# Performance work log

Measured on AMD Instinct MI355X. Metric: run time of the kernel, lower is better.

## Reference

```python
import jax, jax.numpy as jnp
import numpy as np

N = 524288
L = 16          # num_levels
F = 2           # per_level_dim
T = 1 << 19     # hashmap size per level
BASE, MAXR = 32, 2048
SCALE = np.exp(np.log(MAXR / BASE) / (L - 1))
RES = [int(np.floor(BASE * SCALE ** lv)) + 1 for lv in range(L)]
ACTIVE = 4 * F  # init_active_level * per_level_dim (progressive mask)
D_HID = 64
N_FREQS = 6

_P1 = jnp.uint32(2654435761)
_P2 = jnp.uint32(805459861)
_OFF = jnp.array([[(c >> d) & 1 for d in range(3)] for c in range(8)], dtype=jnp.uint32)  # [8,3]


def setup_inputs() -> dict:
    key = jax.random.key(0)
    ks = jax.random.split(key, 8)
    x = (jax.random.uniform(ks[0], (N, 3)) * 2.0 - 1.0) * 0.999  # inside [-bound, bound]
    v = jax.random.normal(ks[1], (N, 3))
    v = v / jnp.linalg.norm(v, axis=-1, keepdims=True)
    o = jax.random.normal(ks[2], (N, 3))  # unused by forward (kept for signature fidelity)
    table = jax.random.uniform(ks[3], (L, T, F), minval=-1e-4, maxval=1e-4)
    d_in = 3 + 3 * 2 * N_FREQS + L * F  # xyz + fourier + hashgrid = 71
    def lin(k, fi, fo):
        return jax.random.normal(k, (fi, fo)) * np.sqrt(2.0 / fi).astype(np.float32)
    dw1 = lin(ks[4], d_in, D_HID); db1 = jnp.zeros((D_HID,), jnp.float32)
    dw2 = lin(ks[5], D_HID, 1 + D_HID); db2 = jnp.zeros((1 + D_HID,), jnp.float32)
    rw1 = lin(ks[6], D_HID + 9, D_HID); rb1 = jnp.zeros((D_HID,), jnp.float32)
    rw2 = lin(ks[7], D_HID, 3); rb2 = jnp.zeros((3,), jnp.float32)
    return dict(x=x, v=v, o=o, table=table, dw1=dw1, db1=db1, dw2=dw2, db2=db2,
                rw1=rw1, rb1=rb1, rw2=rw2, rb2=rb2)


def hashgrid(x01, table):
    """Multi-res hash encoding with Smoothstep interpolation. x01 in [0,1]^3."""
    feats = []
    for lv in range(L):
        pos = x01 * RES[lv]
        p0 = jnp.floor(pos)
        t = pos - p0
        w = t * t * (3.0 - 2.0 * t)                       # smoothstep weights [N,3]
        corner = p0.astype(jnp.uint32)[:, None, :] + _OFF[None]  # [N,8,3]
        h = (corner[..., 0] ^ (corner[..., 1] * _P1) ^ (corner[..., 2] * _P2)) & jnp.uint32(T - 1)
        cw = jnp.prod(jnp.where(_OFF[None] == 1, w[:, None, :], 1.0 - w[:, None, :]), axis=-1)  # [N,8]
        feats.append(jnp.sum(table[lv][h.astype(jnp.int32)] * cw[..., None], axis=1))  # [N,F]
    return jnp.concatenate(feats, axis=-1)  # [N, L*F]


def fourier(x):
    freqs = 2.0 ** jnp.arange(N_FREQS, dtype=x.dtype)  # log-sampled 2^0..2^5
    ang = x[..., None] * freqs                         # [N,3,6]
    return jnp.concatenate([jnp.sin(ang), jnp.cos(ang)], axis=-1).reshape(x.shape[0], -1)


def sh3(d):
    """Spherical harmonics, degree 3 (levels=3) -> 9 features."""
    xx, yy, zz = d[..., 0], d[..., 1], d[..., 2]
    return jnp.stack([
        0.28209479177387814 * jnp.ones_like(xx),
        -0.4886025119029199 * yy, 0.4886025119029199 * zz, -0.4886025119029199 * xx,
        1.0925484305920792 * xx * yy, -1.0925484305920792 * yy * zz,
        0.9461746957575601 * zz * zz - 0.31539156525252005,
        -1.0925484305920792 * xx * zz,
        0.5462742152960396 * (xx * xx - yy * yy)], axis=-1)


def reference(x, v, o, table, dw1, db1, dw2, db2, rw1, rb1, rw2, rb2):
    x01 = (x + 1.0) * 0.5  # bound = 1.0
    grid = hashgrid(x01, table)
    mask = (jnp.arange(L * F) < ACTIVE).astype(grid.dtype)  # progressive level mask
    x_enc = jnp.concatenate([x, fourier(x), grid * mask], axis=-1)  # [N,71]
    h = jax.nn.relu(x_enc @ dw1 + db1)
    dout = h @ dw2 + db2                 # [N, 1 + d_hidden]
    sigma = jnp.exp(dout[..., :1])       # trunc_exp forward == exp
    feat = jax.nn.relu(dout[..., 1:])
    rgb_in = jnp.concatenate([feat, sh3(v)], axis=-1)  # [N, 73]
    hr = jax.nn.relu(rgb_in @ rw1 + rb1)
    rgb = jax.nn.sigmoid(hr @ rw2 + rb2)
    return sigma, rgb
```

## Files before the change

### kernel.cpp

```cpp
#include <hip/hip_runtime.h>

#define NPTS   524288
#define TBLM   ((1u << 19) - 1u)
#define THR    256
#define CHUNK  64
#define CHUNKS 8
#define GRID   (NPTS / (CHUNK * CHUNKS))

typedef _Float16 half8  __attribute__((ext_vector_type(8)));
typedef _Float16 half4v __attribute__((ext_vector_type(4)));
typedef _Float16 half2v __attribute__((ext_vector_type(2)));
typedef float    f32x4  __attribute__((ext_vector_type(4)));


__global__ __launch_bounds__(256)
void prep(const float* __restrict__ dw1, const float* __restrict__ db1,
          const float* __restrict__ dw2, const float* __restrict__ db2,
          const float* __restrict__ rw1, const float* __restrict__ rb1,
          const float* __restrict__ rw2, const float* __restrict__ rb2,
          void* __restrict__ ws)
{
    const int t = blockIdx.x * 256 + threadIdx.x;
    if (t < 16384) {
        float w = 0.0f;
        if (t < 4096) {
            const int u = t, mkc = u >> 9, m = mkc >> 1, kc = mkc & 1;
            const int lane = (u >> 3) & 63, j = u & 7;
            const int row = 16 * m + (lane & 15);
            const int kp  = kc * 32 + (lane >> 4) * 8 + j;
            if (kp < 39)      w = dw1[kp * 64 + row];
            else if (kp == 39) w = 0.0f;
            else if (kp < 48) w = dw1[(kp - 1) * 64 + row];
        } else if (t < 9216) {
            const int u = t - 4096, mkc = u >> 9, m = mkc >> 1, kc = mkc & 1;
            const int lane = (u >> 3) & 63, j = u & 7;
            const int row = 16 * m + (lane & 15);
            const int k   = kc * 32 + (lane >> 4) * 8 + j;
            if (row < 65) w = dw2[k * 65 + row];
        } else if (t < 15360) {
            const int u = t - 9216, mkc = u >> 9, m = mkc / 3, kc = mkc - 3 * m;
            const int lane = (u >> 3) & 63, j = u & 7;
            const int row = 16 * m + (lane & 15);
            const int kp  = kc * 32 + (lane >> 4) * 8 + j;
            if (kp >= 1 && kp <= 73) w = rw1[(kp - 1) * 64 + row];
        } else {
            const int u = t - 15360, kc = u >> 9;
            const int lane = (u >> 3) & 63, j = u & 7;
            const int row = lane & 15;
            const int k   = kc * 32 + (lane >> 4) * 8 + j;
            if (row < 3) w = rw2[k * 3 + row];
        }
        ((_Float16*)ws)[t] = (_Float16)w;
    } else if (t < 16384 + 224) {
        const int u = t - 16384;
        float b = 0.0f;
        if (u < 64)        b = db1[u];
        else if (u < 144)  { const int r = u - 64;  if (r < 65) b = db2[r]; }
        else if (u < 208)  b = rb1[u - 144];
        else               { const int r = u - 208; if (r < 3)  b = rb2[r]; }
        ((float*)((char*)ws + 32768))[u] = b;
    }
}

__device__ __forceinline__ float sstep(float t) { return t * t * (3.0f - 2.0f * t); }

struct GS {
    float  x0, x1, x2, v0, v1, v2;
    float  ax, ay, az;
    float2 t0, t1, t2, t3, t4, t5, t6, t7;
};

__device__ __forceinline__ void gather_issue(int gi, int role,
    const float* __restrict__ x, const float* __restrict__ v,
    const float* __restrict__ table, GS& s)
{
    s.x0 = x[3 * gi + 0]; s.x1 = x[3 * gi + 1]; s.x2 = x[3 * gi + 2];
    if (role == 1) { s.v0 = v[3 * gi + 0]; s.v1 = v[3 * gi + 1]; s.v2 = v[3 * gi + 2]; }
    const float rf = (role == 0) ? 33.f : (role == 1) ? 43.f : (role == 2) ? 56.f : 74.f;
    const float u0 = (s.x0 + 1.f) * 0.5f, u1 = (s.x1 + 1.f) * 0.5f, u2 = (s.x2 + 1.f) * 0.5f;
    const float px = u0 * rf, py = u1 * rf, pz = u2 * rf;
    const float fx = floorf(px), fy = floorf(py), fz = floorf(pz);
    s.ax = sstep(px - fx); s.ay = sstep(py - fy); s.az = sstep(pz - fz);
    const unsigned cx = (unsigned)fx, cy = (unsigned)fy, cz = (unsigned)fz;
    const float* tb = table + (unsigned)role * (TBLM + 1u) * 2u;
    const unsigned hy0 = cy * 2654435761u, hy1 = (cy + 1u) * 2654435761u;
    const unsigned hz0 = cz * 805459861u,  hz1 = (cz + 1u) * 805459861u;
#define LDC(dst, HX, HY, HZ) { const unsigned hh = ((HX) ^ (HY) ^ (HZ)) & TBLM; \
                               dst = *reinterpret_cast<const float2*>(tb + hh * 2u); }
    LDC(s.t0, cx,      hy0, hz0);
    LDC(s.t1, cx + 1u, hy0, hz0);
    LDC(s.t2, cx,      hy1, hz0);
    LDC(s.t3, cx + 1u, hy1, hz0);
    LDC(s.t4, cx,      hy0, hz1);
    LDC(s.t5, cx + 1u, hy0, hz1);
    LDC(s.t6, cx,      hy1, hz1);
    LDC(s.t7, cx + 1u, hy1, hz1);
#undef LDC
}

__device__ __forceinline__ void encode_finish(const GS& s, int role, _Float16* row)
{
    const float ax = s.ax, ay = s.ay, az = s.az;
    const float bx = 1.f - ax, by = 1.f - ay, bz = 1.f - az;
    const float p00 = bx * by, p10 = ax * by, p01 = bx * ay, p11 = ax * ay;
    const float w0 = p00 * bz, w1 = p10 * bz, w2 = p01 * bz, w3 = p11 * bz;
    const float w4 = p00 * az, w5 = p10 * az, w6 = p01 * az, w7 = p11 * az;
    float g0 = w0 * s.t0.x, g1 = w0 * s.t0.y;
    g0 = fmaf(w1, s.t1.x, g0); g1 = fmaf(w1, s.t1.y, g1);
    g0 = fmaf(w2, s.t2.x, g0); g1 = fmaf(w2, s.t2.y, g1);
    g0 = fmaf(w3, s.t3.x, g0); g1 = fmaf(w3, s.t3.y, g1);
    g0 = fmaf(w4, s.t4.x, g0); g1 = fmaf(w4, s.t4.y, g1);
    g0 = fmaf(w5, s.t5.x, g0); g1 = fmaf(w5, s.t5.y, g1);
    g0 = fmaf(w6, s.t6.x, g0); g1 = fmaf(w6, s.t6.y, g1);
    g0 = fmaf(w7, s.t7.x, g0); g1 = fmaf(w7, s.t7.y, g1);
    half2v gh; gh[0] = (_Float16)g0; gh[1] = (_Float16)g1;
    *(half2v*)(row + 40 + 2 * role) = gh;

    if (role == 0) {
        float e[40];
        e[0] = s.x0; e[1] = s.x1; e[2] = s.x2;
        const float a[3] = {s.x0, s.x1, s.x2};
        #pragma unroll
        for (int d = 0; d < 3; ++d)
            #pragma unroll
            for (int f = 0; f < 6; ++f) {
                const float ang = a[d] * (float)(1 << f);
                e[3 + d * 12 + f]     = __sinf(ang);
                e[3 + d * 12 + 6 + f] = __cosf(ang);
            }
        e[39] = 0.0f;
        #pragma unroll
        for (int chk = 0; chk < 5; ++chk) {
            half8 h;
            #pragma unroll
            for (int i = 0; i < 8; ++i) h[i] = (_Float16)e[chk * 8 + i];
            *(half8*)(row + chk * 8) = h;
        }
    } else if (role == 1) {
        const float v0 = s.v0, v1 = s.v1, v2 = s.v2;
        float sh[9];
        sh[0] = 0.28209479177387814f;
        sh[1] = -0.4886025119029199f * v1;
        sh[2] =  0.4886025119029199f * v2;
        sh[3] = -0.4886025119029199f * v0;
        sh[4] =  1.0925484305920792f * v0 * v1;
        sh[5] = -1.0925484305920792f * v1 * v2;
        sh[6] =  0.9461746957575601f * v2 * v2 - 0.31539156525252005f;
        sh[7] = -1.0925484305920792f * v0 * v2;
        sh[8] =  0.5462742152960396f * (v0 * v0 - v1 * v1);
        half8 s0, s1;
        s0[0] = (_Float16)0.f;
        #pragma unroll
        for (int i = 0; i < 7; ++i) s0[i + 1] = (_Float16)sh[i];
        s1[0] = (_Float16)sh[7]; s1[1] = (_Float16)sh[8];
        #pragma unroll
        for (int i = 2; i < 8; ++i) s1[i] = (_Float16)0.f;
        *(half8*)(row + 64) = s0;
        *(half8*)(row + 72) = s1;
    }
}

__global__ __launch_bounds__(THR, 2)
void nerf_fwd(const float* __restrict__ x,
              const float* __restrict__ v,
              const float* __restrict__ table,
              const float* __restrict__ ws,
              float* __restrict__ out)
{
    __shared__ __align__(16) unsigned char smem[23424];
    float*    sbias = (float*)smem;
    _Float16* aB    = (_Float16*)(smem + 896);
    _Float16* bB    = (_Float16*)(smem + 14208);

    const int tid  = threadIdx.x;
    const int lane = tid & 63;
    const int wv   = tid >> 6;
    const int lr   = lane & 15;
    const int lg   = lane >> 4;
    const int role = lane & 3;
    const int ep   = (wv << 4) + (lane >> 2);
    const int gi0  = blockIdx.x * (CHUNK * CHUNKS);

    GS cur, nxt;
    gather_issue(gi0 + ep, role, x, v, table, cur);

    const _Float16* wsH = (const _Float16*)ws;
    half8 W1[4][2], W2[5][2], W3[4][3], W4[2];
    #pragma unroll
    for (int m = 0; m < 4; ++m)
        #pragma unroll
        for (int kc = 0; kc < 2; ++kc)
            W1[m][kc] = *(const half8*)(wsH + (m * 2 + kc) * 512 + lane * 8);
    #pragma unroll
    for (int m = 0; m < 5; ++m)
        #pragma unroll
        for (int kc = 0; kc < 2; ++kc)
            W2[m][kc] = *(const half8*)(wsH + 4096 + (m * 2 + kc) * 512 + lane * 8);
    #pragma unroll
    for (int m = 0; m < 4; ++m)
        #pragma unroll
        for (int kc = 0; kc < 3; ++kc)
            W3[m][kc] = *(const half8*)(wsH + 9216 + (m * 3 + kc) * 512 + lane * 8);
    #pragma unroll
    for (int kc = 0; kc < 2; ++kc)
        W4[kc] = *(const half8*)(wsH + 15360 + kc * 512 + lane * 8);

    if (tid < 56) ((uint4*)sbias)[tid] = ((const uint4*)((const char*)ws + 32768))[tid];
    __syncthreads();

    {
        _Float16* rowp = aB + ep * 104;
        half8 z;
        #pragma unroll
        for (int i = 0; i < 8; ++i) z[i] = (_Float16)0.f;
        *(half8*)(rowp + 48 + 8 * role) = z;
        if (role < 2) *(half8*)(rowp + 80 + 8 * role) = z;
    }

    const int pt = (wv << 4) + lr;

    #pragma unroll 2
    for (int c = 0; c < CHUNKS; ++c) {
        const int cbase = gi0 + c * CHUNK;

        encode_finish(cur, role, aB + ep * 104);

        if (c + 1 < CHUNKS)
            gather_issue(gi0 + (c + 1) * CHUNK + ep, role, x, v, table, nxt);

        {
            const half8 B0 = *(const half8*)(aB + pt * 104 + 0 * 32 + lg * 8);
            const half8 B1 = *(const half8*)(aB + pt * 104 + 1 * 32 + lg * 8);
            #pragma unroll
            for (int m = 0; m < 4; ++m) {
                f32x4 cr = *(const f32x4*)(sbias + 0 + m * 16 + 4 * lg);
                cr = __builtin_amdgcn_mfma_f32_16x16x32_f16(W1[m][0], B0, cr, 0, 0, 0);
                cr = __builtin_amdgcn_mfma_f32_16x16x32_f16(W1[m][1], B1, cr, 0, 0, 0);
                half4v o4;
                #pragma unroll
                for (int r = 0; r < 4; ++r) o4[r] = (_Float16)fmaxf(cr[r], 0.f);
                *(half4v*)(bB + pt * 72 + 16 * m + 4 * lg) = o4;
            }
        }

        {
            const half8 B0 = *(const half8*)(bB + pt * 72 + 0 * 32 + lg * 8);
            const half8 B1 = *(const half8*)(bB + pt * 72 + 1 * 32 + lg * 8);
            #pragma unroll
            for (int m = 0; m < 4; ++m) {
                f32x4 cr = *(const f32x4*)(sbias + 64 + m * 16 + 4 * lg);
                cr = __builtin_amdgcn_mfma_f32_16x16x32_f16(W2[m][0], B0, cr, 0, 0, 0);
                cr = __builtin_amdgcn_mfma_f32_16x16x32_f16(W2[m][1], B1, cr, 0, 0, 0);
                half4v o4;
                #pragma unroll
                for (int r = 0; r < 4; ++r) o4[r] = (_Float16)fmaxf(cr[r], 0.f);
                *(half4v*)(aB + pt * 104 + 16 * m + 4 * lg) = o4;
                if (m == 0 && lg == 0)
                    out[cbase + pt] = __expf(cr[0]);
            }
            {
                f32x4 cr = *(const f32x4*)(sbias + 64 + 4 * 16 + 4 * lg);
                cr = __builtin_amdgcn_mfma_f32_16x16x32_f16(W2[4][0], B0, cr, 0, 0, 0);
                cr = __builtin_amdgcn_mfma_f32_16x16x32_f16(W2[4][1], B1, cr, 0, 0, 0);
                if (lg == 0) aB[pt * 104 + 64] = (_Float16)fmaxf(cr[0], 0.f);
            }
        }

        {
            const half8 B0 = *(const half8*)(aB + pt * 104 + 0 * 32 + lg * 8);
            const half8 B1 = *(const half8*)(aB + pt * 104 + 1 * 32 + lg * 8);
            const half8 B2 = *(const half8*)(aB + pt * 104 + 2 * 32 + lg * 8);
            #pragma unroll
            for (int m = 0; m < 4; ++m) {
                f32x4 cr = *(const f32x4*)(sbias + 144 + m * 16 + 4 * lg);
                cr = __builtin_amdgcn_mfma_f32_16x16x32_f16(W3[m][0], B0, cr, 0, 0, 0);
                cr = __builtin_amdgcn_mfma_f32_16x16x32_f16(W3[m][1], B1, cr, 0, 0, 0);
                cr = __builtin_amdgcn_mfma_f32_16x16x32_f16(W3[m][2], B2, cr, 0, 0, 0);
                half4v o4;
                #pragma unroll
                for (int r = 0; r < 4; ++r) o4[r] = (_Float16)fmaxf(cr[r], 0.f);
                *(half4v*)(bB + pt * 72 + 16 * m + 4 * lg) = o4;
            }
        }

        {
            const half8 B0 = *(const half8*)(bB + pt * 72 + 0 * 32 + lg * 8);
            const half8 B1 = *(const half8*)(bB + pt * 72 + 1 * 32 + lg * 8);
            f32x4 cr = *(const f32x4*)(sbias + 208 + 4 * lg);
            cr = __builtin_amdgcn_mfma_f32_16x16x32_f16(W4[0], B0, cr, 0, 0, 0);
            cr = __builtin_amdgcn_mfma_f32_16x16x32_f16(W4[1], B1, cr, 0, 0, 0);
            if (lg == 0) {
                const int gpt = cbase + pt;
                #pragma unroll
                for (int r = 0; r < 3; ++r)
                    out[NPTS + 3 * gpt + r] = 1.0f / (1.0f + __expf(-cr[r]));
            }
        }

        if (c + 1 < CHUNKS) cur = nxt;
    }
}

extern "C" void kernel_launch(void* const* d_in, const int* in_sizes, int n_in,
                              void* d_out, int out_size, void* d_ws, size_t ws_size,
                              hipStream_t stream) {
    const float* x     = (const float*)d_in[0];
    const float* v     = (const float*)d_in[1];
    const float* table = (const float*)d_in[3];
    const float* dw1   = (const float*)d_in[4];
    const float* db1   = (const float*)d_in[5];
    const float* dw2   = (const float*)d_in[6];
    const float* db2   = (const float*)d_in[7];
    const float* rw1   = (const float*)d_in[8];
    const float* rb1   = (const float*)d_in[9];
    const float* rw2   = (const float*)d_in[10];
    const float* rb2   = (const float*)d_in[11];
    float* out = (float*)d_out;

    hipLaunchKernelGGL(prep, dim3(65), dim3(256), 0, stream,
                       dw1, db1, dw2, db2, rw1, rb1, rw2, rb2, d_ws);
    hipLaunchKernelGGL(nerf_fwd, dim3(GRID), dim3(THR), 0, stream,
                       x, v, table, (const float*)d_ws, out);
}
```

Measured before the change: 194.9 us.

## Encode directly into MFMA B registers, fp16 table copy, per-lane-group encoding

Drops the LDS staging of the encoding row. Each lane group now builds its own MFMA B fragments: Fourier features via double-angle recurrences, the hash-grid level for that group, and the raw xyz. The first-layer weights are permuted to match this layout. Layer 2's extra output and the SH features are injected straight into the third B fragment in registers, and CHUNKS is halved. When workspace allows, it also converts the active hash-table levels to fp16 each call to halve gather bytes. This adds a 2048-block conversion pass that reads about 16MB per call, and the recurrence adds some approximation error.

```diff
diff --git a/kernel.cpp b/kernel.cpp
--- a/kernel.cpp
+++ b/kernel.cpp
@@ -4,8 +4,10 @@
 #define TBLM   ((1u << 19) - 1u)
 #define THR    256
 #define CHUNK  64
-#define CHUNKS 8
+#define CHUNKS 4
 #define GRID   (NPTS / (CHUNK * CHUNKS))
+#define TAB16_OFF   36864u
+#define TAB16_BYTES (4u * 524288u * 2u * 2u)
 
 typedef _Float16 half8  __attribute__((ext_vector_type(8)));
 typedef _Float16 half4v __attribute__((ext_vector_type(4)));
@@ -18,148 +20,159 @@
           const float* __restrict__ dw2, const float* __restrict__ db2,
           const float* __restrict__ rw1, const float* __restrict__ rb1,
           const float* __restrict__ rw2, const float* __restrict__ rb2,
-          void* __restrict__ ws)
+          const float* __restrict__ table, void* __restrict__ ws, int doTab)
 {
-    const int t = blockIdx.x * 256 + threadIdx.x;
-    if (t < 16384) {
-        float w = 0.0f;
-        if (t < 4096) {
-            const int u = t, mkc = u >> 9, m = mkc >> 1, kc = mkc & 1;
-            const int lane = (u >> 3) & 63, j = u & 7;
-            const int row = 16 * m + (lane & 15);
-            const int kp  = kc * 32 + (lane >> 4) * 8 + j;
-            if (kp < 39)      w = dw1[kp * 64 + row];
-            else if (kp == 39) w = 0.0f;
-            else if (kp < 48) w = dw1[(kp - 1) * 64 + row];
-        } else if (t < 9216) {
-            const int u = t - 4096, mkc = u >> 9, m = mkc >> 1, kc = mkc & 1;
-            const int lane = (u >> 3) & 63, j = u & 7;
-            const int row = 16 * m + (lane & 15);
-            const int k   = kc * 32 + (lane >> 4) * 8 + j;
-            if (row < 65) w = dw2[k * 65 + row];
-        } else if (t < 15360) {
-            const int u = t - 9216, mkc = u >> 9, m = mkc / 3, kc = mkc - 3 * m;
-            const int lane = (u >> 3) & 63, j = u & 7;
-            const int row = 16 * m + (lane & 15);
-            const int kp  = kc * 32 + (lane >> 4) * 8 + j;
-            if (kp >= 1 && kp <= 73) w = rw1[(kp - 1) * 64 + row];
-        } else {
-            const int u = t - 15360, kc = u >> 9;
-            const int lane = (u >> 3) & 63, j = u & 7;
-            const int row = lane & 15;
-            const int k   = kc * 32 + (lane >> 4) * 8 + j;
-            if (row < 3) w = rw2[k * 3 + row];
-        }
-        ((_Float16*)ws)[t] = (_Float16)w;
-    } else if (t < 16384 + 224) {
-        const int u = t - 16384;
-        float b = 0.0f;
-        if (u < 64)        b = db1[u];
-        else if (u < 144)  { const int r = u - 64;  if (r < 65) b = db2[r]; }
-        else if (u < 208)  b = rb1[u - 144];
-        else               { const int r = u - 208; if (r < 3)  b = rb2[r]; }
-        ((float*)((char*)ws + 32768))[u] = b;
+    const int b = blockIdx.x;
+    if (b < 65) {
+        const int t = b * 256 + threadIdx.x;
+        if (t < 16384) {
+            float w = 0.0f;
+            if (t < 4096) {
+                const int u = t, mkc = u >> 9, m = mkc >> 1, kc = mkc & 1;
+                const int lane = (u >> 3) & 63, j = u & 7;
+                const int row = 16 * m + (lane & 15);
+                const int kp  = kc * 32 + (lane >> 4) * 8 + j;
+                const int g = (kp >> 3) & 3, i = ((kp >> 5) << 3) | (kp & 7);
+                int ri = -1;
+                if (i < 6)        ri = (g < 3) ? 3 + 12 * g + i : -1;
+                else if (i < 12)  ri = (g < 3) ? 3 + 12 * g + 6 + (i - 6) : -1;
+                else if (i == 12) ri = 39 + 2 * g;
+                else if (i == 13) ri = 40 + 2 * g;
+                else if (i == 14) ri = (g == 0) ? 0 : ((g == 3) ? 2 : -1);
+                else              ri = (g == 0) ? 1 : -1;
+                w = (ri >= 0) ? dw1[ri * 64 + row] : 0.0f;
+            } else if (t < 9216) {
+                const int u = t - 4096, mkc = u >> 9, m = mkc >> 1, kc = mkc & 1;
+                const int lane = (u >> 3) & 63, j = u & 7;
+                const int row = 16 * m + (lane & 15);
+                const int k   = kc * 32 + (lane >> 4) * 8 + j;
+                if (row < 65) w = dw2[k * 65 + row];
+            } else if (t < 15360) {
+                const int u = t - 9216, mkc = u >> 9, m = mkc / 3, kc = mkc - 3 * m;
+                const int lane = (u >> 3) & 63, j = u & 7;
+                const int row = 16 * m + (lane & 15);
+                const int kp  = kc * 32 + (lane >> 4) * 8 + j;
+                if (kp >= 1 && kp <= 73) w = rw1[(kp - 1) * 64 + row];
+            } else {
+                const int u = t - 15360, kc = u >> 9;
+                const int lane = (u >> 3) & 63, j = u & 7;
+                const int row = lane & 15;
+                const int k   = kc * 32 + (lane >> 4) * 8 + j;
+                if (row < 3) w = rw2[k * 3 + row];
+            }
+            ((_Float16*)ws)[t] = (_Float16)w;
+        } else if (t < 16384 + 224) {
+            const int u = t - 16384;
+            float bv = 0.0f;
+            if (u < 64)        bv = db1[u];
+            else if (u < 144)  { const int r = u - 64;  if (r < 65) bv = db2[r]; }
+            else if (u < 208)  bv = rb1[u - 144];
+            else               { const int r = u - 208; if (r < 3)  bv = rb2[r]; }
+            ((float*)((char*)ws + 32768))[u] = bv;
+        }
+    } else if (doTab) {
+        const int t2 = (b - 65) * 256 + (int)threadIdx.x;
+        const float4* src = (const float4*)(table + (size_t)t2 * 8);
+        const float4 f0 = src[0], f1 = src[1];
+        half8 h;
+        h[0] = (_Float16)f0.x; h[1] = (_Float16)f0.y; h[2] = (_Float16)f0.z; h[3] = (_Float16)f0.w;
+        h[4] = (_Float16)f1.x; h[5] = (_Float16)f1.y; h[6] = (_Float16)f1.z; h[7] = (_Float16)f1.w;
+        *(half8*)((_Float16*)((char*)ws + TAB16_OFF) + (size_t)t2 * 8) = h;
     }
 }
 
 __device__ __forceinline__ float sstep(float t) { return t * t * (3.0f - 2.0f * t); }
 
 struct GS {
-    float  x0, x1, x2, v0, v1, v2;
-    float  ax, ay, az;
-    float2 t0, t1, t2, t3, t4, t5, t6, t7;
+    float x0, x1, x2, v0, v1, v2;
+    float ax, ay, az;
+    float2 f0, f1, f2, f3, f4, f5, f6, f7;
+    unsigned h0, h1, h2, h3, h4, h5, h6, h7;
 };
 
-__device__ __forceinline__ void gather_issue(int gi, int role,
+template<bool F16T>
+__device__ __forceinline__ void gather_issue(int gi, int lg,
     const float* __restrict__ x, const float* __restrict__ v,
-    const float* __restrict__ table, GS& s)
+    const float* __restrict__ tab32, const _Float16* __restrict__ tab16, GS& s)
 {
     s.x0 = x[3 * gi + 0]; s.x1 = x[3 * gi + 1]; s.x2 = x[3 * gi + 2];
-    if (role == 1) { s.v0 = v[3 * gi + 0]; s.v1 = v[3 * gi + 1]; s.v2 = v[3 * gi + 2]; }
-    const float rf = (role == 0) ? 33.f : (role == 1) ? 43.f : (role == 2) ? 56.f : 74.f;
-    const float u0 = (s.x0 + 1.f) * 0.5f, u1 = (s.x1 + 1.f) * 0.5f, u2 = (s.x2 + 1.f) * 0.5f;
-    const float px = u0 * rf, py = u1 * rf, pz = u2 * rf;
+    s.v0 = v[3 * gi + 0]; s.v1 = v[3 * gi + 1]; s.v2 = v[3 * gi + 2];
+    const float rf = (lg == 0) ? 33.f : (lg == 1) ? 43.f : (lg == 2) ? 56.f : 74.f;
+    const float px = (s.x0 + 1.f) * 0.5f * rf;
+    const float py = (s.x1 + 1.f) * 0.5f * rf;
+    const float pz = (s.x2 + 1.f) * 0.5f * rf;
     const float fx = floorf(px), fy = floorf(py), fz = floorf(pz);
     s.ax = sstep(px - fx); s.ay = sstep(py - fy); s.az = sstep(pz - fz);
     const unsigned cx = (unsigned)fx, cy = (unsigned)fy, cz = (unsigned)fz;
-    const float* tb = table + (unsigned)role * (TBLM + 1u) * 2u;
     const unsigned hy0 = cy * 2654435761u, hy1 = (cy + 1u) * 2654435761u;
     const unsigned hz0 = cz * 805459861u,  hz1 = (cz + 1u) * 805459861u;
-#define LDC(dst, HX, HY, HZ) { const unsigned hh = ((HX) ^ (HY) ^ (HZ)) & TBLM; \
+    if (F16T) {
+        const _Float16* tb = tab16 + (unsigned)lg * ((TBLM + 1u) * 2u);
+#define LDH(dst, HX, HY, HZ) { const unsigned hh = ((HX) ^ (HY) ^ (HZ)) & TBLM; \
+                               dst = *reinterpret_cast<const unsigned*>(tb + hh * 2u); }
+        LDH(s.h0, cx,      hy0, hz0); LDH(s.h1, cx + 1u, hy0, hz0);
+        LDH(s.h2, cx,      hy1, hz0); LDH(s.h3, cx + 1u, hy1, hz0);
+        LDH(s.h4, cx,      hy0, hz1); LDH(s.h5, cx + 1u, hy0, hz1);
+        LDH(s.h6, cx,      hy1, hz1); LDH(s.h7, cx + 1u, hy1, hz1);
+#undef LDH
+    } else {
+        const float* tb = tab32 + (unsigned)lg * ((TBLM + 1u) * 2u);
+#define LDF(dst, HX, HY, HZ) { const unsigned hh = ((HX) ^ (HY) ^ (HZ)) & TBLM; \
                                dst = *reinterpret_cast<const float2*>(tb + hh * 2u); }
-    LDC(s.t0, cx,      hy0, hz0);
-    LDC(s.t1, cx + 1u, hy0, hz0);
-    LDC(s.t2, cx,      hy1, hz0);
-    LDC(s.t3, cx + 1u, hy1, hz0);
-    LDC(s.t4, cx,      hy0, hz1);
-    LDC(s.t5, cx + 1u, hy0, hz1);
-    LDC(s.t6, cx,      hy1, hz1);
-    LDC(s.t7, cx + 1u, hy1, hz1);
-#undef LDC
-}
-
-__device__ __forceinline__ void encode_finish(const GS& s, int role, _Float16* row)
+        LDF(s.f0, cx,      hy0, hz0); LDF(s.f1, cx + 1u, hy0, hz0);
+        LDF(s.f2, cx,      hy1, hz0); LDF(s.f3, cx + 1u, hy1, hz0);
+        LDF(s.f4, cx,      hy0, hz1); LDF(s.f5, cx + 1u, hy0, hz1);
+        LDF(s.f6, cx,      hy1, hz1); LDF(s.f7, cx + 1u, hy1, hz1);
+#undef LDF
+    }
+}
+
+template<bool F16T>
+__device__ __forceinline__ void build_B01(const GS& s, int lg, half8& B0, half8& B1)
 {
     const float ax = s.ax, ay = s.ay, az = s.az;
     const float bx = 1.f - ax, by = 1.f - ay, bz = 1.f - az;
     const float p00 = bx * by, p10 = ax * by, p01 = bx * ay, p11 = ax * ay;
     const float w0 = p00 * bz, w1 = p10 * bz, w2 = p01 * bz, w3 = p11 * bz;
     const float w4 = p00 * az, w5 = p10 * az, w6 = p01 * az, w7 = p11 * az;
-    float g0 = w0 * s.t0.x, g1 = w0 * s.t0.y;
-    g0 = fmaf(w1, s.t1.x, g0); g1 = fmaf(w1, s.t1.y, g1);
-    g0 = fmaf(w2, s.t2.x, g0); g1 = fmaf(w2, s.t2.y, g1);
-    g0 = fmaf(w3, s.t3.x, g0); g1 = fmaf(w3, s.t3.y, g1);
-    g0 = fmaf(w4, s.t4.x, g0); g1 = fmaf(w4, s.t4.y, g1);
-    g0 = fmaf(w5, s.t5.x, g0); g1 = fmaf(w5, s.t5.y, g1);
-    g0 = fmaf(w6, s.t6.x, g0); g1 = fmaf(w6, s.t6.y, g1);
-    g0 = fmaf(w7, s.t7.x, g0); g1 = fmaf(w7, s.t7.y, g1);
-    half2v gh; gh[0] = (_Float16)g0; gh[1] = (_Float16)g1;
-    *(half2v*)(row + 40 + 2 * role) = gh;
-
-    if (role == 0) {
-        float e[40];
-        e[0] = s.x0; e[1] = s.x1; e[2] = s.x2;
-        const float a[3] = {s.x0, s.x1, s.x2};
-        #pragma unroll
-        for (int d = 0; d < 3; ++d)
-            #pragma unroll
-            for (int f = 0; f < 6; ++f) {
-                const float ang = a[d] * (float)(1 << f);
-                e[3 + d * 12 + f]     = __sinf(ang);
-                e[3 + d * 12 + 6 + f] = __cosf(ang);
-            }
-        e[39] = 0.0f;
-        #pragma unroll
-        for (int chk = 0; chk < 5; ++chk) {
-            half8 h;
-            #pragma unroll
-            for (int i = 0; i < 8; ++i) h[i] = (_Float16)e[chk * 8 + i];
-            *(half8*)(row + chk * 8) = h;
-        }
-    } else if (role == 1) {
-        const float v0 = s.v0, v1 = s.v1, v2 = s.v2;
-        float sh[9];
-        sh[0] = 0.28209479177387814f;
-        sh[1] = -0.4886025119029199f * v1;
-        sh[2] =  0.4886025119029199f * v2;
-        sh[3] = -0.4886025119029199f * v0;
-        sh[4] =  1.0925484305920792f * v0 * v1;
-        sh[5] = -1.0925484305920792f * v1 * v2;
-        sh[6] =  0.9461746957575601f * v2 * v2 - 0.31539156525252005f;
-        sh[7] = -1.0925484305920792f * v0 * v2;
-        sh[8] =  0.5462742152960396f * (v0 * v0 - v1 * v1);
-        half8 s0, s1;
-        s0[0] = (_Float16)0.f;
-        #pragma unroll
-        for (int i = 0; i < 7; ++i) s0[i + 1] = (_Float16)sh[i];
-        s1[0] = (_Float16)sh[7]; s1[1] = (_Float16)sh[8];
-        #pragma unroll
-        for (int i = 2; i < 8; ++i) s1[i] = (_Float16)0.f;
-        *(half8*)(row + 64) = s0;
-        *(half8*)(row + 72) = s1;
-    }
-}
-
+    float e0[8], e1[8];
+    if (F16T) {
+        const unsigned hv[8] = {s.h0, s.h1, s.h2, s.h3, s.h4, s.h5, s.h6, s.h7};
+        #pragma unroll
+        for (int i = 0; i < 8; ++i) {
+            const half2v h = __builtin_bit_cast(half2v, hv[i]);
+            e0[i] = (float)h[0]; e1[i] = (float)h[1];
+        }
+    } else {
+        const float2 fv[8] = {s.f0, s.f1, s.f2, s.f3, s.f4, s.f5, s.f6, s.f7};
+        #pragma unroll
+        for (int i = 0; i < 8; ++i) { e0[i] = fv[i].x; e1[i] = fv[i].y; }
+    }
+    const float wts[8] = {w0, w1, w2, w3, w4, w5, w6, w7};
+    float glo = 0.f, ghi = 0.f;
+    #pragma unroll
+    for (int i = 0; i < 8; ++i) { glo = fmaf(wts[i], e0[i], glo); ghi = fmaf(wts[i], e1[i], ghi); }
+
+    const float a = (lg == 0) ? s.x0 : (lg == 1) ? s.x1 : s.x2;
+    float sv[6], cv[6];
+    sv[0] = __sinf(a); cv[0] = __cosf(a);
+    #pragma unroll
+    for (int f = 1; f < 6; ++f) {
+        const float ss = sv[f - 1], cc = cv[f - 1];
+        sv[f] = 2.f * ss * cc;
+        cv[f] = fmaf(-2.f * ss, ss, 1.f);
+    }
+    const float ex0 = (lg == 0) ? s.x0 : s.x2;
+    const float ex1 = s.x1;
+    B0[0] = (_Float16)sv[0]; B0[1] = (_Float16)sv[1]; B0[2] = (_Float16)sv[2];
+    B0[3] = (_Float16)sv[3]; B0[4] = (_Float16)sv[4]; B0[5] = (_Float16)sv[5];
+    B0[6] = (_Float16)cv[0]; B0[7] = (_Float16)cv[1];
+    B1[0] = (_Float16)cv[2]; B1[1] = (_Float16)cv[3]; B1[2] = (_Float16)cv[4];
+    B1[3] = (_Float16)cv[5]; B1[4] = (_Float16)glo;   B1[5] = (_Float16)ghi;
+    B1[6] = (_Float16)ex0;   B1[7] = (_Float16)ex1;
+}
+
+template<bool F16T>
 __global__ __launch_bounds__(THR, 2)
 void nerf_fwd(const float* __restrict__ x,
               const float* __restrict__ v,
@@ -167,22 +180,21 @@
               const float* __restrict__ ws,
               float* __restrict__ out)
 {
-    __shared__ __align__(16) unsigned char smem[23424];
+    __shared__ __align__(16) unsigned char smem[10112];
     float*    sbias = (float*)smem;
-    _Float16* aB    = (_Float16*)(smem + 896);
-    _Float16* bB    = (_Float16*)(smem + 14208);
+    _Float16* bB    = (_Float16*)(smem + 896);
 
     const int tid  = threadIdx.x;
     const int lane = tid & 63;
     const int wv   = tid >> 6;
     const int lr   = lane & 15;
     const int lg   = lane >> 4;
-    const int role = lane & 3;
-    const int ep   = (wv << 4) + (lane >> 2);
+    const int pt   = (wv << 4) + lr;
     const int gi0  = blockIdx.x * (CHUNK * CHUNKS);
+    const _Float16* tab16 = (const _Float16*)((const char*)ws + TAB16_OFF);
 
     GS cur, nxt;
-    gather_issue(gi0 + ep, role, x, v, table, cur);
+    gather_issue<F16T>(gi0 + pt, lg, x, v, table, tab16, cur);
 
     const _Float16* wsH = (const _Float16*)ws;
     half8 W1[4][2], W2[5][2], W3[4][3], W4[2];
@@ -207,74 +219,79 @@
 
     if (tid < 56) ((uint4*)sbias)[tid] = ((const uint4*)((const char*)ws + 32768))[tid];
     __syncthreads();
-
-    {
-        _Float16* rowp = aB + ep * 104;
-        half8 z;
-        #pragma unroll
-        for (int i = 0; i < 8; ++i) z[i] = (_Float16)0.f;
-        *(half8*)(rowp + 48 + 8 * role) = z;
-        if (role < 2) *(half8*)(rowp + 80 + 8 * role) = z;
-    }
-
-    const int pt = (wv << 4) + lr;
 
     #pragma unroll 2
     for (int c = 0; c < CHUNKS; ++c) {
         const int cbase = gi0 + c * CHUNK;
 
-        encode_finish(cur, role, aB + ep * 104);
+        half8 B0, B1;
+        build_B01<F16T>(cur, lg, B0, B1);
 
         if (c + 1 < CHUNKS)
-            gather_issue(gi0 + (c + 1) * CHUNK + ep, role, x, v, table, nxt);
-
+            gather_issue<F16T>(gi0 + (c + 1) * CHUNK + pt, lg, x, v, table, tab16, nxt);
+
+        #pragma unroll
+        for (int m = 0; m < 4; ++m) {
+            f32x4 cr = *(const f32x4*)(sbias + 0 + m * 16 + 4 * lg);
+            cr = __builtin_amdgcn_mfma_f32_16x16x32_f16(W1[m][0], B0, cr, 0, 0, 0);
+            cr = __builtin_amdgcn_mfma_f32_16x16x32_f16(W1[m][1], B1, cr, 0, 0, 0);
+            half4v o4;
+            #pragma unroll
+            for (int r = 0; r < 4; ++r) o4[r] = (_Float16)fmaxf(cr[r], 0.f);
+            *(half4v*)(bB + pt * 72 + 16 * m + 4 * lg) = o4;
+        }
+
+        float f63;
         {
-            const half8 B0 = *(const half8*)(aB + pt * 104 + 0 * 32 + lg * 8);
-            const half8 B1 = *(const half8*)(aB + pt * 104 + 1 * 32 + lg * 8);
+            const half8 C0 = *(const half8*)(bB + pt * 72 + 0 * 32 + lg * 8);
+            const half8 C1 = *(const half8*)(bB + pt * 72 + 1 * 32 + lg * 8);
             #pragma unroll
             for (int m = 0; m < 4; ++m) {
-                f32x4 cr = *(const f32x4*)(sbias + 0 + m * 16 + 4 * lg);
-                cr = __builtin_amdgcn_mfma_f32_16x16x32_f16(W1[m][0], B0, cr, 0, 0, 0);
-                cr = __builtin_amdgcn_mfma_f32_16x16x32_f16(W1[m][1], B1, cr, 0, 0, 0);
+                f32x4 cr = *(const f32x4*)(sbias + 64 + m * 16 + 4 * lg);
+                cr = __builtin_amdgcn_mfma_f32_16x16x32_f16(W2[m][0], C0, cr, 0, 0, 0);
+                cr = __builtin_amdgcn_mfma_f32_16x16x32_f16(W2[m][1], C1, cr, 0, 0, 0);
                 half4v o4;
                 #pragma unroll
                 for (int r = 0; r < 4; ++r) o4[r] = (_Float16)fmaxf(cr[r], 0.f);
                 *(half4v*)(bB + pt * 72 + 16 * m + 4 * lg) = o4;
-            }
-        }
-
-        {
-            const half8 B0 = *(const half8*)(bB + pt * 72 + 0 * 32 + lg * 8);
-            const half8 B1 = *(const half8*)(bB + pt * 72 + 1 * 32 + lg * 8);
-            #pragma unroll
-            for (int m = 0; m < 4; ++m) {
-                f32x4 cr = *(const f32x4*)(sbias + 64 + m * 16 + 4 * lg);
-                cr = __builtin_amdgcn_mfma_f32_16x16x32_f16(W2[m][0], B0, cr, 0, 0, 0);
-                cr = __builtin_amdgcn_mfma_f32_16x16x32_f16(W2[m][1], B1, cr, 0, 0, 0);
-                half4v o4;
-                #pragma unroll
-                for (int r = 0; r < 4; ++r) o4[r] = (_Float16)fmaxf(cr[r], 0.f);
-                *(half4v*)(aB + pt * 104 + 16 * m + 4 * lg) = o4;
                 if (m == 0 && lg == 0)
                     out[cbase + pt] = __expf(cr[0]);
             }
-            {
-                f32x4 cr = *(const f32x4*)(sbias + 64 + 4 * 16 + 4 * lg);
-                cr = __builtin_amdgcn_mfma_f32_16x16x32_f16(W2[4][0], B0, cr, 0, 0, 0);
-                cr = __builtin_amdgcn_mfma_f32_16x16x32_f16(W2[4][1], B1, cr, 0, 0, 0);
-                if (lg == 0) aB[pt * 104 + 64] = (_Float16)fmaxf(cr[0], 0.f);
-            }
+            f32x4 cr = *(const f32x4*)(sbias + 64 + 4 * 16 + 4 * lg);
+            cr = __builtin_amdgcn_mfma_f32_16x16x32_f16(W2[4][0], C0, cr, 0, 0, 0);
+            cr = __builtin_amdgcn_mfma_f32_16x16x32_f16(W2[4][1], C1, cr, 0, 0, 0);
+            f63 = fmaxf(cr[0], 0.f);
         }
 
         {
-            const half8 B0 = *(const half8*)(aB + pt * 104 + 0 * 32 + lg * 8);
-            const half8 B1 = *(const half8*)(aB + pt * 104 + 1 * 32 + lg * 8);
-            const half8 B2 = *(const half8*)(aB + pt * 104 + 2 * 32 + lg * 8);
+            const float v0 = cur.v0, v1 = cur.v1, v2 = cur.v2;
+            const float sh0 = 0.28209479177387814f;
+            const float sh1 = -0.4886025119029199f * v1;
+            const float sh2 =  0.4886025119029199f * v2;
+            const float sh3v = -0.4886025119029199f * v0;
+            const float sh4 =  1.0925484305920792f * v0 * v1;
+            const float sh5 = -1.0925484305920792f * v1 * v2;
+            const float sh6 =  0.9461746957575601f * v2 * v2 - 0.31539156525252005f;
+            const float sh7 = -1.0925484305920792f * v0 * v2;
+            const float sh8 =  0.5462742152960396f * (v0 * v0 - v1 * v1);
+            const bool g0 = (lg == 0), g1 = (lg == 1);
+            half8 B2;
+            B2[0] = (_Float16)(g0 ? f63 : (g1 ? sh7 : 0.f));
+            B2[1] = (_Float16)(g0 ? sh0 : (g1 ? sh8 : 0.f));
+            B2[2] = (_Float16)(g0 ? sh1 : 0.f);
+            B2[3] = (_Float16)(g0 ? sh2 : 0.f);
+            B2[4] = (_Float16)(g0 ? sh3v : 0.f);
+            B2[5] = (_Float16)(g0 ? sh4 : 0.f);
+            B2[6] = (_Float16)(g0 ? sh5 : 0.f);
+            B2[7] = (_Float16)(g0 ? sh6 : 0.f);
+
+            const half8 C0 = *(const half8*)(bB + pt * 72 + 0 * 32 + lg * 8);
+            const half8 C1 = *(const half8*)(bB + pt * 72 + 1 * 32 + lg * 8);
             #pragma unroll
             for (int m = 0; m < 4; ++m) {
                 f32x4 cr = *(const f32x4*)(sbias + 144 + m * 16 + 4 * lg);
-                cr = __builtin_amdgcn_mfma_f32_16x16x32_f16(W3[m][0], B0, cr, 0, 0, 0);
-                cr = __builtin_amdgcn_mfma_f32_16x16x32_f16(W3[m][1], B1, cr, 0, 0, 0);
+                cr = __builtin_amdgcn_mfma_f32_16x16x32_f16(W3[m][0], C0, cr, 0, 0, 0);
+                cr = __builtin_amdgcn_mfma_f32_16x16x32_f16(W3[m][1], C1, cr, 0, 0, 0);
                 cr = __builtin_amdgcn_mfma_f32_16x16x32_f16(W3[m][2], B2, cr, 0, 0, 0);
                 half4v o4;
                 #pragma unroll
@@ -284,11 +301,11 @@
         }
 
         {
-            const half8 B0 = *(const half8*)(bB + pt * 72 + 0 * 32 + lg * 8);
-            const half8 B1 = *(const half8*)(bB + pt * 72 + 1 * 32 + lg * 8);
+            const half8 C0 = *(const half8*)(bB + pt * 72 + 0 * 32 + lg * 8);
+            const half8 C1 = *(const half8*)(bB + pt * 72 + 1 * 32 + lg * 8);
             f32x4 cr = *(const f32x4*)(sbias + 208 + 4 * lg);
-            cr = __builtin_amdgcn_mfma_f32_16x16x32_f16(W4[0], B0, cr, 0, 0, 0);
-            cr = __builtin_amdgcn_mfma_f32_16x16x32_f16(W4[1], B1, cr, 0, 0, 0);
+            cr = __builtin_amdgcn_mfma_f32_16x16x32_f16(W4[0], C0, cr, 0, 0, 0);
+            cr = __builtin_amdgcn_mfma_f32_16x16x32_f16(W4[1], C1, cr, 0, 0, 0);
             if (lg == 0) {
                 const int gpt = cbase + pt;
                 #pragma unroll
@@ -317,8 +334,15 @@
     const float* rb2   = (const float*)d_in[11];
     float* out = (float*)d_out;
 
-    hipLaunchKernelGGL(prep, dim3(65), dim3(256), 0, stream,
-                       dw1, db1, dw2, db2, rw1, rb1, rw2, rb2, d_ws);
-    hipLaunchKernelGGL(nerf_fwd, dim3(GRID), dim3(THR), 0, stream,
-                       x, v, table, (const float*)d_ws, out);
-}
+    const bool useF16 = (ws_size >= (size_t)TAB16_OFF + TAB16_BYTES);
+    const int prepBlocks = useF16 ? (65 + 2048) : 65;
+    hipLaunchKernelGGL(prep, dim3(prepBlocks), dim3(256), 0, stream,
+                       dw1, db1, dw2, db2, rw1, rb1, rw2, rb2, table, d_ws,
+                       useF16 ? 1 : 0);
+    if (useF16)
+        hipLaunchKernelGGL((nerf_fwd<true>), dim3(GRID), dim3(THR), 0, stream,
+                           x, v, table, (const float*)d_ws, out);
+    else
+        hipLaunchKernelGGL((nerf_fwd<false>), dim3(GRID), dim3(THR), 0, stream,
+                           x, v, table, (const float*)d_ws, out);
+}
```

Measured after the change: 182.7 us. 1.07x faster.
